# Performance work log

Hardware: AMD Instinct MI355X
Metric: run time of the kernel (lower is better)

The kernel has to match this reference:

```python
import jax, jax.numpy as jnp
import numpy as np


def setup_inputs() -> dict:
    key = jax.random.key(0)
    ks = jax.random.split(key, 8)
    Dm, E, N, R, K = 1024, 2048, 16, 64, 3
    s = 0.02
    x = jax.random.normal(ks[0], (2, 2048, Dm), jnp.float32)
    W_in = jax.random.normal(ks[1], (2 * E, Dm), jnp.float32) * s
    conv_w = jax.random.normal(ks[2], (E, 1, K), jnp.float32) * 0.1
    conv_b = jnp.zeros((E,), jnp.float32)
    W_sel = jax.random.normal(ks[3], (R + 2 * N, E), jnp.float32) * s
    dt_w = jax.random.normal(ks[4], (E, R), jnp.float32) * (R ** -0.5)
    dt_b = jax.random.normal(ks[5], (E,), jnp.float32) * 0.5
    A_log = jnp.log(jnp.tile(jnp.arange(1, N + 1, dtype=jnp.float32)[None, :], (E, 1)))
    D_param = jnp.ones((E,), jnp.float32)
    W_out = jax.random.normal(ks[6], (Dm, E), jnp.float32) * s
    return dict(x=x, W_in=W_in, conv_w=conv_w, conv_b=conv_b, W_sel=W_sel,
                dt_w=dt_w, dt_b=dt_b, A_log=A_log, D_param=D_param, W_out=W_out)


def reference(x, W_in, conv_w, conv_b, W_sel, dt_w, dt_b, A_log, D_param, W_out):
    Bsz, L, Dm = x.shape
    E = W_in.shape[0] // 2
    N = A_log.shape[1]
    R = dt_w.shape[1]
    K = conv_w.shape[-1]

    # input projection -> x, z
    xz = jnp.einsum('bld,ed->ble', x, W_in)          # [B,L,2E]
    xc, z = jnp.split(xz, 2, axis=-1)                # [B,L,E] each

    # causal depthwise conv1d + SiLU
    xt = xc.transpose(0, 2, 1)                       # [B,E,L]
    u = jax.lax.conv_general_dilated(
        xt, conv_w, window_strides=(1,), padding=[(K - 1, 0)],
        feature_group_count=E, dimension_numbers=('NCH', 'OIH', 'NCH'))
    u = jax.nn.silu(u + conv_b[None, :, None]).transpose(0, 2, 1)  # [B,L,E]

    # selective projection -> dt (low rank), B, C
    dbc = jnp.einsum('ble,re->blr', u, W_sel)        # [B,L,R+2N]
    dt_low, Bm, Cm = jnp.split(dbc, [R, R + N], axis=-1)
    delta = jax.nn.softplus(jnp.einsum('blr,er->ble', dt_low, dt_w) + dt_b)  # [B,L,E]

    A = -jnp.exp(A_log)                              # [E,N]

    def step(h, inp):
        d_t, u_t, B_t, C_t = inp                     # [B,E],[B,E],[B,N],[B,N]
        dA = jnp.exp(d_t[..., None] * A)             # [B,E,N]
        h = dA * h + (d_t * u_t)[..., None] * B_t[:, None, :]
        y_t = jnp.einsum('ben,bn->be', h, C_t)
        return h, y_t

    h0 = jnp.zeros((Bsz, E, N), x.dtype)
    seq = (delta.transpose(1, 0, 2), u.transpose(1, 0, 2),
           Bm.transpose(1, 0, 2), Cm.transpose(1, 0, 2))
    _, ys = jax.lax.scan(step, h0, seq)              # ys: [L,B,E]

    y = ys.transpose(1, 0, 2) + u * D_param          # skip term D*u
    y = y * jax.nn.silu(z)                           # gating
    return jnp.einsum('ble,de->bld', y, W_out)       # [B,L,Dm]
```

## Files before the change

### kernel.cpp

```cpp
#include <hip/hip_runtime.h>
#include <cstdint>
#include <cstddef>

typedef unsigned short ushort_t;
typedef __bf16 bf16x8 __attribute__((ext_vector_type(8)));
typedef float f32x4 __attribute__((ext_vector_type(4)));
typedef unsigned short us8v __attribute__((ext_vector_type(8)));

#define TSZ   4096
#define LSEQ  2048
#define DM    1024
#define EE    2048
#define NST   16
#define RR    64
#define NC    64
#define CL    32
#define BE    4096
#define NSPLIT 16
#define NSPLIT4 2

__device__ __forceinline__ ushort_t f2bf(float f) {
  uint32_t u = __builtin_bit_cast(uint32_t, f);
  u = (u + 0x7FFFu + ((u >> 16) & 1u)) >> 16;
  return (ushort_t)u;
}
__device__ __forceinline__ float bf2f(ushort_t h) {
  uint32_t u = ((uint32_t)h) << 16;
  return __builtin_bit_cast(float, u);
}

__device__ __forceinline__ size_t paddr(int r, int k, int logK) {
  return ((size_t)(r >> 7) << (7 + logK)) + (size_t)(((k >> 5) << 12) +
         (((k >> 3) & 3) << 10) + ((r & 127) << 3) + (k & 7));
}
__device__ __forceinline__ size_t src_of(int j, int logK) {
  int rt = j >> (7 + logK);
  int rem = j & ((1 << (7 + logK)) - 1);
  int kp = rem >> 12;
  int kc = (rem >> 10) & 3;
  int rr = (rem >> 3) & 127;
  int k0 = rem & 7;
  return ((size_t)(rt * 128 + rr) << logK) + (kp << 5) + (kc << 3) + k0;
}

#define NX_  (TSZ * DM)
#define NWI_ (2 * EE * DM)
#define NDT_ (EE * RR)
#define NWO_ (DM * EE)
#define NWS_ (128 * EE)
#define NCVT (NX_ + NWI_ + NDT_ + NWO_ + NWS_)

__device__ __forceinline__ void cvt8(const float* __restrict__ src, ushort_t* __restrict__ dst,
                                     int j, int logK) {
  size_t s = src_of(j, logK);
  float4 a = *(const float4*)(src + s);
  float4 b = *(const float4*)(src + s + 4);
  us8v v;
  v[0] = f2bf(a.x); v[1] = f2bf(a.y); v[2] = f2bf(a.z); v[3] = f2bf(a.w);
  v[4] = f2bf(b.x); v[5] = f2bf(b.y); v[6] = f2bf(b.z); v[7] = f2bf(b.w);
  *(us8v*)(dst + j) = v;
}

__global__ void cvt_all_kernel(const float* __restrict__ x, const float* __restrict__ W_in,
                               const float* __restrict__ dt_w, const float* __restrict__ W_out,
                               const float* __restrict__ W_sel,
                               ushort_t* __restrict__ xb, ushort_t* __restrict__ wib,
                               ushort_t* __restrict__ dtwb, ushort_t* __restrict__ woutb,
                               ushort_t* __restrict__ wselb) {
  int j = (blockIdx.x * 256 + threadIdx.x) * 8;
  if (j < NX_) { cvt8(x, xb, j, 10); return; }
  j -= NX_;
  if (j < NWI_) { cvt8(W_in, wib, j, 10); return; }
  j -= NWI_;
  if (j < NDT_) { cvt8(dt_w, dtwb, j, 6); return; }
  j -= NDT_;
  if (j < NWO_) { cvt8(W_out, woutb, j, 11); return; }
  j -= NWO_;
  if (j < NWS_) {
    size_t s = src_of(j, 11);
    int row = (int)(s >> 11);
    us8v v;
    if (row < 96) {
      float4 a = *(const float4*)(W_sel + s);
      float4 b = *(const float4*)(W_sel + s + 4);
      v[0] = f2bf(a.x); v[1] = f2bf(a.y); v[2] = f2bf(a.z); v[3] = f2bf(a.w);
      v[4] = f2bf(b.x); v[5] = f2bf(b.y); v[6] = f2bf(b.z); v[7] = f2bf(b.w);
    } else {
      v = (us8v)0;
    }
    *(us8v*)(wselb + j) = v;
  }
}

__device__ __forceinline__ void stage4(const ushort_t* g, ushort_t* lds, int tid) {
#pragma unroll
  for (int s = 0; s < 4; s++)
    __builtin_amdgcn_global_load_lds(
        (const __attribute__((address_space(1))) unsigned int*)(g + (tid + 256 * s) * 8),
        (__attribute__((address_space(3))) unsigned int*)(lds + (tid + 256 * s) * 8), 16, 0, 0);
}

__global__ __launch_bounds__(256) void gemm_bt2_kernel(
    const ushort_t* __restrict__ A, const ushort_t* __restrict__ B, int K, int ksplit,
    float* __restrict__ Cf, int ldcf, ushort_t* __restrict__ Cb, int ldcb,
    const float* __restrict__ bias, int nvalid, int mode) {
  __shared__ __align__(16) ushort_t lA[2][128 * 64];
  const int tid = threadIdx.x;
  const int mtile = blockIdx.x, ntile = blockIdx.y;

  const size_t abase = (size_t)mtile * 128 * K;
  const size_t bbase = (size_t)ntile * 128 * K;
  const int lane = tid & 63, w = tid >> 6;
  const int wm = (w >> 1) * 64, wn = (w & 1) * 64;
  const int lr = lane & 15, quad = lane >> 4;

  auto loadB = [&](bf16x8 (&dst)[2][4], const ushort_t* pbase) {
#pragma unroll
    for (int kk = 0; kk < 2; kk++)
#pragma unroll
      for (int ni = 0; ni < 4; ni++)
        dst[kk][ni] = *(const bf16x8*)(pbase + (size_t)(kk * 512 + quad * 128 + wn + ni * 16 + lr) * 8);
  };

  f32x4 acc[4][4];
#pragma unroll
  for (int i = 0; i < 4; i++)
#pragma unroll
    for (int j = 0; j < 4; j++) acc[i][j] = (f32x4){0.f, 0.f, 0.f, 0.f};

  const int kstart = blockIdx.z * ksplit;
  const int nIter = (ksplit ? ksplit : K) >> 6;

  stage4(A + abase + (size_t)kstart * 128, lA[0], tid);
  bf16x8 bcur[2][4];
  loadB(bcur, B + bbase + (size_t)kstart * 128);

#pragma unroll 2
  for (int i = 0; i < nIter; ++i) {
    const int knext = (i + 1 < nIter) ? (kstart + (i + 1) * 64) : kstart;
    __asm__ volatile("s_barrier" ::: "memory");
    stage4(A + abase + (size_t)knext * 128, lA[(i + 1) & 1], tid);
    bf16x8 bnx[2][4];
    loadB(bnx, B + bbase + (size_t)knext * 128);
    __asm__ volatile("s_waitcnt vmcnt(12)" ::: "memory");
    __asm__ volatile("s_barrier" ::: "memory");
    const ushort_t* lab = lA[i & 1];
#pragma unroll
    for (int kk = 0; kk < 2; kk++) {
      bf16x8 af[4];
#pragma unroll
      for (int mi = 0; mi < 4; mi++)
        af[mi] = *(const bf16x8*)&lab[(kk * 512 + quad * 128 + wm + mi * 16 + lr) * 8];
#pragma unroll
      for (int mi = 0; mi < 4; mi++)
#pragma unroll
        for (int ni = 0; ni < 4; ni++)
          acc[mi][ni] = __builtin_amdgcn_mfma_f32_16x16x32_bf16(af[mi], bcur[kk][ni], acc[mi][ni], 0, 0, 0);
    }
#pragma unroll
    for (int kk = 0; kk < 2; kk++)
#pragma unroll
      for (int ni = 0; ni < 4; ni++)
        bcur[kk][ni] = bnx[kk][ni];
  }
  __asm__ volatile("s_waitcnt vmcnt(0)" ::: "memory");

  float* Cfp = (mode == 4) ? (Cf + (size_t)blockIdx.z * TSZ * ldcf) : Cf;
  const int grow0 = mtile * 128 + wm + quad * 4;
  const int gcol0 = ntile * 128 + wn + lr;
#pragma unroll
  for (int mi = 0; mi < 4; mi++) {
#pragma unroll
    for (int ni = 0; ni < 4; ni++) {
      int gcol = gcol0 + ni * 16;
      if (gcol >= nvalid) continue;
#pragma unroll
      for (int reg = 0; reg < 4; reg++) {
        int grow = grow0 + mi * 16 + reg;
        float v = acc[mi][ni][reg];
        if (mode == 1) {
          Cb[(size_t)grow * ldcb + gcol] = f2bf(v);
        } else if (mode == 5) {
          float t = v + bias[gcol];
          float sp = fmaxf(t, 0.f) + __logf(1.f + __expf(-fabsf(t)));
          ((_Float16*)Cb)[(size_t)grow * ldcb + gcol] = (_Float16)sp;
        } else if (mode == 6) {
          atomicAdd(&Cf[(size_t)grow * ldcf + gcol], v);
        } else {
          Cfp[(size_t)grow * ldcf + gcol] = v;
        }
      }
    }
  }
}

__global__ void reduce_dbc_kernel(const float* __restrict__ pbuf,
                                  float* __restrict__ bcbuf, ushort_t* __restrict__ dtlb) {
  int i = blockIdx.x * 256 + threadIdx.x;
  int t = i >> 7, col = i & 127;
  if (col >= 96) return;
  float s = 0.f;
#pragma unroll
  for (int p = 0; p < NSPLIT; p++) s += pbuf[(size_t)p * TSZ * 128 + i];
  if (col < 64) dtlb[paddr(t, col, 6)] = f2bf(s);
  else bcbuf[(size_t)t * 32 + (col - 64)] = s;
}

__global__ void conv_silu_kernel(const ushort_t* __restrict__ xzb,
                                 const float* __restrict__ conv_w,
                                 const float* __restrict__ conv_b,
                                 ushort_t* __restrict__ ub) {
  int j = (blockIdx.x * 256 + threadIdx.x) * 8;
  int rt = j >> 18;
  int rem = j & 262143;
  int e0 = ((rem >> 12) << 5) + (((rem >> 10) & 3) << 3);
  int t = rt * 128 + ((rem >> 3) & 127);
  int l = t & (LSEQ - 1);
  const ushort_t* r2 = xzb + (size_t)t * 4096 + e0;
  us8v x2 = *(const us8v*)r2;
  float acc[8];
#pragma unroll
  for (int q = 0; q < 8; q++)
    acc[q] = fmaf(conv_w[(e0 + q) * 3 + 2], bf2f(x2[q]), conv_b[e0 + q]);
  if (l >= 1) {
    us8v x1 = *(const us8v*)(r2 - 4096);
#pragma unroll
    for (int q = 0; q < 8; q++) acc[q] = fmaf(conv_w[(e0 + q) * 3 + 1], bf2f(x1[q]), acc[q]);
  }
  if (l >= 2) {
    us8v x0 = *(const us8v*)(r2 - 8192);
#pragma unroll
    for (int q = 0; q < 8; q++) acc[q] = fmaf(conv_w[(e0 + q) * 3 + 0], bf2f(x0[q]), acc[q]);
  }
  us8v o;
#pragma unroll
  for (int q = 0; q < 8; q++) {
    float s = acc[q] / (1.f + __expf(-acc[q]));
    o[q] = f2bf(s);
  }
  *(us8v*)(ub + j) = o;
}

__global__ void scan_passA_kernel(const _Float16* __restrict__ delta,
                                  const ushort_t* __restrict__ ub,
                                  const float* __restrict__ bcbuf,
                                  _Float16* __restrict__ chunk_h,
                                  float* __restrict__ chunk_sd) {
  const int c = blockIdx.y;
  const int bblk = blockIdx.x >> 3;
  const int tg0 = bblk * LSEQ + c * CL;
  const int be = blockIdx.x * 256 + threadIdx.x;
  const int e = be & (EE - 1);
  float h[NST];
#pragma unroll
  for (int n = 0; n < NST; n++) h[n] = 0.f;
  float sd = 0.f;
  size_t ub0 = paddr(tg0, e, 11);
  const float* __restrict__ bcrow = bcbuf + (size_t)tg0 * 32;
  for (int i = 0; i < CL; i++) {
    int tg = tg0 + i;
    float d = (float)delta[(size_t)tg * EE + e];
    float u = bf2f(ub[ub0 + i * 8]);
    float Bn[NST];
    *(float4*)&Bn[0]  = *(const float4*)(bcrow + 0);
    *(float4*)&Bn[4]  = *(const float4*)(bcrow + 4);
    *(float4*)&Bn[8]  = *(const float4*)(bcrow + 8);
    *(float4*)&Bn[12] = *(const float4*)(bcrow + 12);
    bcrow += 32;
    float r = __expf(-d);
    float wdu = d * u;
    float p = 1.f;
#pragma unroll
    for (int n = 0; n < NST; n++) {
      p *= r;
      h[n] = fmaf(p, h[n], wdu * Bn[n]);
    }
    sd += d;
  }
  size_t o = ((size_t)c * BE + be) * NST;
#pragma unroll
  for (int n = 0; n < NST; n++) chunk_h[o + n] = (_Float16)h[n];
  chunk_sd[(size_t)c * BE + be] = sd;
}

__global__ void combine_kernel(const _Float16* __restrict__ chunk_h,
                               const float* __restrict__ chunk_sd,
                               _Float16* __restrict__ hstart) {
  int gid = blockIdx.x * 256 + threadIdx.x;
  int be = gid >> 4, n = gid & 15;
  float hs = 0.f;
  float np1 = (float)(n + 1);
  for (int c = 0; c < NC; c++) {
    hstart[(size_t)c * BE * NST + gid] = (_Float16)hs;
    float sdv = chunk_sd[c * BE + be];
    float P = __expf(-np1 * sdv);
    hs = fmaf(P, hs, (float)chunk_h[(size_t)c * BE * NST + gid]);
  }
}

__global__ void scan_passC_kernel(const _Float16* __restrict__ delta,
                                  const ushort_t* __restrict__ ub,
                                  const ushort_t* __restrict__ xzb,
                                  const float* __restrict__ bcbuf,
                                  const _Float16* __restrict__ hstart,
                                  const float* __restrict__ D_param,
                                  ushort_t* __restrict__ gated) {
  const int c = blockIdx.y;
  const int bblk = blockIdx.x >> 3;
  const int tg0 = bblk * LSEQ + c * CL;
  const int be = blockIdx.x * 256 + threadIdx.x;
  const int e = be & (EE - 1);
  float h[NST];
  size_t ho = ((size_t)c * BE + be) * NST;
#pragma unroll
  for (int n = 0; n < NST; n++) h[n] = (float)hstart[ho + n];
  float Dp = D_param[e];
  size_t pk0 = paddr(tg0, e, 11);
  const float* __restrict__ bcrow = bcbuf + (size_t)tg0 * 32;
  for (int i = 0; i < CL; i++) {
    int tg = tg0 + i;
    float d = (float)delta[(size_t)tg * EE + e];
    float u = bf2f(ub[pk0 + i * 8]);
    float z = bf2f(xzb[(size_t)tg * 4096 + 2048 + e]);
    float Bn[NST], Cn[NST];
    *(float4*)&Bn[0]  = *(const float4*)(bcrow + 0);
    *(float4*)&Bn[4]  = *(const float4*)(bcrow + 4);
    *(float4*)&Bn[8]  = *(const float4*)(bcrow + 8);
    *(float4*)&Bn[12] = *(const float4*)(bcrow + 12);
    *(float4*)&Cn[0]  = *(const float4*)(bcrow + 16);
    *(float4*)&Cn[4]  = *(const float4*)(bcrow + 20);
    *(float4*)&Cn[8]  = *(const float4*)(bcrow + 24);
    *(float4*)&Cn[12] = *(const float4*)(bcrow + 28);
    bcrow += 32;
    float r = __expf(-d);
    float wdu = d * u;
    float p = 1.f, y = 0.f;
#pragma unroll
    for (int n = 0; n < NST; n++) {
      p *= r;
      h[n] = fmaf(p, h[n], wdu * Bn[n]);
      y = fmaf(h[n], Cn[n], y);
    }
    y = fmaf(u, Dp, y);
    float sz = z / (1.f + __expf(-z));
    gated[pk0 + i * 8] = f2bf(y * sz);
  }
}

extern "C" void kernel_launch(void* const* d_in, const int* in_sizes, int n_in,
                              void* d_out, int out_size, void* d_ws, size_t ws_size,
                              hipStream_t stream) {
  const float* x       = (const float*)d_in[0];
  const float* W_in    = (const float*)d_in[1];
  const float* conv_w  = (const float*)d_in[2];
  const float* conv_b  = (const float*)d_in[3];
  const float* W_sel   = (const float*)d_in[4];
  const float* dt_w    = (const float*)d_in[5];
  const float* dt_b    = (const float*)d_in[6];
  const float* D_param = (const float*)d_in[8];
  const float* W_out   = (const float*)d_in[9];
  float* out = (float*)d_out;

  char* ws = (char*)d_ws;
  size_t off = 0;
  auto alloc = [&](size_t bytes) -> void* {
    void* p = ws + off;
    off += (bytes + 255) & ~(size_t)255;
    return p;
  };
  ushort_t* xzb   = (ushort_t*)alloc((size_t)TSZ * 4096 * 2);
  ushort_t* ubuf  = (ushort_t*)alloc((size_t)TSZ * EE * 2);
  ushort_t* wselb = (ushort_t*)alloc((size_t)128 * EE * 2);
  ushort_t* dtwb  = (ushort_t*)alloc((size_t)EE * RR * 2);
  ushort_t* woutb = (ushort_t*)alloc((size_t)DM * EE * 2);
  float*    bcbuf = (float*)alloc((size_t)TSZ * 32 * 4);
  ushort_t* dtlb  = (ushort_t*)alloc((size_t)TSZ * RR * 2);
  float*    dscr  = (float*)alloc((size_t)TSZ * EE * 4);
  float*    csd   = (float*)alloc((size_t)NC * BE * 4);
  ushort_t* gated = (ushort_t*)alloc((size_t)TSZ * EE * 2);
  ushort_t* xb    = (ushort_t*)alloc((size_t)TSZ * DM * 2);
  ushort_t* wib   = (ushort_t*)alloc((size_t)(2 * EE) * DM * 2);
  _Float16* delta = (_Float16*)dscr;
  _Float16* chunk_h = (_Float16*)gated;
  _Float16* hstart  = (_Float16*)wib;
  float* pbuf2   = dscr;

  hipMemsetAsync(out, 0, (size_t)TSZ * DM * 4, stream);

  cvt_all_kernel<<<(NCVT / 8 + 255) / 256, 256, 0, stream>>>(x, W_in, dt_w, W_out, W_sel,
                                                             xb, wib, dtwb, woutb, wselb);

  gemm_bt2_kernel<<<dim3(32, 32), 256, 0, stream>>>(
      xb, wib, DM, 0, nullptr, 0, xzb, 4096, nullptr, 4096, 1);

  conv_silu_kernel<<<(TSZ * EE / 8) / 256, 256, 0, stream>>>(xzb, conv_w, conv_b, ubuf);

  gemm_bt2_kernel<<<dim3(32, 1, NSPLIT), 256, 0, stream>>>(
      ubuf, wselb, EE, EE / NSPLIT, pbuf2, 128, nullptr, 0, nullptr, 96, 4);
  reduce_dbc_kernel<<<(TSZ * 128) / 256, 256, 0, stream>>>(pbuf2, bcbuf, dtlb);

  gemm_bt2_kernel<<<dim3(32, 16), 256, 0, stream>>>(
      dtlb, dtwb, RR, 0, nullptr, 0, (ushort_t*)delta, EE, dt_b, EE, 5);

  scan_passA_kernel<<<dim3(BE / 256, NC), 256, 0, stream>>>(delta, ubuf, bcbuf, chunk_h, csd);
  combine_kernel<<<(BE * NST) / 256, 256, 0, stream>>>(chunk_h, csd, hstart);
  scan_passC_kernel<<<dim3(BE / 256, NC), 256, 0, stream>>>(delta, ubuf, xzb, bcbuf, hstart,
                                                            D_param, gated);

  gemm_bt2_kernel<<<dim3(32, 8, NSPLIT4), 256, 0, stream>>>(
      gated, woutb, EE, EE / NSPLIT4, out, DM, nullptr, 0, nullptr, DM, 6);
}
```

Measured before the change: 323.9 us.

## Replace atomic split-K output with partial buffers and reduction kernel; halve dbc split

```diff
diff --git a/kernel.cpp b/kernel.cpp
--- a/kernel.cpp
+++ b/kernel.cpp
@@ -16,7 +16,7 @@
 #define NC    64
 #define CL    32
 #define BE    4096
-#define NSPLIT 16
+#define NSPLIT 8
 #define NSPLIT4 2
 
 __device__ __forceinline__ ushort_t f2bf(float f) {
@@ -100,7 +100,7 @@
         (__attribute__((address_space(3))) unsigned int*)(lds + (tid + 256 * s) * 8), 16, 0, 0);
 }
 
-__global__ __launch_bounds__(256) void gemm_bt2_kernel(
+__global__ __launch_bounds__(256) void gemm_pipe_kernel(
     const ushort_t* __restrict__ A, const ushort_t* __restrict__ B, int K, int ksplit,
     float* __restrict__ Cf, int ldcf, ushort_t* __restrict__ Cb, int ldcb,
     const float* __restrict__ bias, int nvalid, int mode) {
@@ -114,12 +114,13 @@
   const int wm = (w >> 1) * 64, wn = (w & 1) * 64;
   const int lr = lane & 15, quad = lane >> 4;
 
-  auto loadB = [&](bf16x8 (&dst)[2][4], const ushort_t* pbase) {
+  bf16x8 breg[2][2][4];
+  auto loadB = [&](int buf, const ushort_t* pbase) {
 #pragma unroll
     for (int kk = 0; kk < 2; kk++)
 #pragma unroll
       for (int ni = 0; ni < 4; ni++)
-        dst[kk][ni] = *(const bf16x8*)(pbase + (size_t)(kk * 512 + quad * 128 + wn + ni * 16 + lr) * 8);
+        breg[buf][kk][ni] = *(const bf16x8*)(pbase + (size_t)(kk * 512 + quad * 128 + wn + ni * 16 + lr) * 8);
   };
 
   f32x4 acc[4][4];
@@ -132,16 +133,14 @@
   const int nIter = (ksplit ? ksplit : K) >> 6;
 
   stage4(A + abase + (size_t)kstart * 128, lA[0], tid);
-  bf16x8 bcur[2][4];
-  loadB(bcur, B + bbase + (size_t)kstart * 128);
+  loadB(0, B + bbase + (size_t)kstart * 128);
 
 #pragma unroll 2
   for (int i = 0; i < nIter; ++i) {
     const int knext = (i + 1 < nIter) ? (kstart + (i + 1) * 64) : kstart;
     __asm__ volatile("s_barrier" ::: "memory");
     stage4(A + abase + (size_t)knext * 128, lA[(i + 1) & 1], tid);
-    bf16x8 bnx[2][4];
-    loadB(bnx, B + bbase + (size_t)knext * 128);
+    loadB((i + 1) & 1, B + bbase + (size_t)knext * 128);
     __asm__ volatile("s_waitcnt vmcnt(12)" ::: "memory");
     __asm__ volatile("s_barrier" ::: "memory");
     const ushort_t* lab = lA[i & 1];
@@ -155,13 +154,8 @@
       for (int mi = 0; mi < 4; mi++)
 #pragma unroll
         for (int ni = 0; ni < 4; ni++)
-          acc[mi][ni] = __builtin_amdgcn_mfma_f32_16x16x32_bf16(af[mi], bcur[kk][ni], acc[mi][ni], 0, 0, 0);
+          acc[mi][ni] = __builtin_amdgcn_mfma_f32_16x16x32_bf16(af[mi], breg[i & 1][kk][ni], acc[mi][ni], 0, 0, 0);
     }
-#pragma unroll
-    for (int kk = 0; kk < 2; kk++)
-#pragma unroll
-      for (int ni = 0; ni < 4; ni++)
-        bcur[kk][ni] = bnx[kk][ni];
   }
   __asm__ volatile("s_waitcnt vmcnt(0)" ::: "memory");
 
@@ -184,8 +178,6 @@
           float t = v + bias[gcol];
           float sp = fmaxf(t, 0.f) + __logf(1.f + __expf(-fabsf(t)));
           ((_Float16*)Cb)[(size_t)grow * ldcb + gcol] = (_Float16)sp;
-        } else if (mode == 6) {
-          atomicAdd(&Cf[(size_t)grow * ldcf + gcol], v);
         } else {
           Cfp[(size_t)grow * ldcf + gcol] = v;
         }
@@ -204,6 +196,14 @@
   for (int p = 0; p < NSPLIT; p++) s += pbuf[(size_t)p * TSZ * 128 + i];
   if (col < 64) dtlb[paddr(t, col, 6)] = f2bf(s);
   else bcbuf[(size_t)t * 32 + (col - 64)] = s;
+}
+
+__global__ void reduce_out_kernel(const float* __restrict__ pbuf, float* __restrict__ out) {
+  int i = blockIdx.x * 256 + threadIdx.x;
+  float s = pbuf[i];
+#pragma unroll
+  for (int p = 1; p < NSPLIT4; p++) s += pbuf[(size_t)p * TSZ * DM + i];
+  out[i] = s;
 }
 
 __global__ void conv_silu_kernel(const ushort_t* __restrict__ xzb,
@@ -384,22 +384,21 @@
   _Float16* chunk_h = (_Float16*)gated;
   _Float16* hstart  = (_Float16*)wib;
   float* pbuf2   = dscr;
-
-  hipMemsetAsync(out, 0, (size_t)TSZ * DM * 4, stream);
+  float* pbuf4   = dscr;
 
   cvt_all_kernel<<<(NCVT / 8 + 255) / 256, 256, 0, stream>>>(x, W_in, dt_w, W_out, W_sel,
                                                              xb, wib, dtwb, woutb, wselb);
 
-  gemm_bt2_kernel<<<dim3(32, 32), 256, 0, stream>>>(
+  gemm_pipe_kernel<<<dim3(32, 32), 256, 0, stream>>>(
       xb, wib, DM, 0, nullptr, 0, xzb, 4096, nullptr, 4096, 1);
 
   conv_silu_kernel<<<(TSZ * EE / 8) / 256, 256, 0, stream>>>(xzb, conv_w, conv_b, ubuf);
 
-  gemm_bt2_kernel<<<dim3(32, 1, NSPLIT), 256, 0, stream>>>(
+  gemm_pipe_kernel<<<dim3(32, 1, NSPLIT), 256, 0, stream>>>(
       ubuf, wselb, EE, EE / NSPLIT, pbuf2, 128, nullptr, 0, nullptr, 96, 4);
   reduce_dbc_kernel<<<(TSZ * 128) / 256, 256, 0, stream>>>(pbuf2, bcbuf, dtlb);
 
-  gemm_bt2_kernel<<<dim3(32, 16), 256, 0, stream>>>(
+  gemm_pipe_kernel<<<dim3(32, 16), 256, 0, stream>>>(
       dtlb, dtwb, RR, 0, nullptr, 0, (ushort_t*)delta, EE, dt_b, EE, 5);
 
   scan_passA_kernel<<<dim3(BE / 256, NC), 256, 0, stream>>>(delta, ubuf, bcbuf, chunk_h, csd);
@@ -407,6 +406,7 @@
   scan_passC_kernel<<<dim3(BE / 256, NC), 256, 0, stream>>>(delta, ubuf, xzb, bcbuf, hstart,
                                                             D_param, gated);
 
-  gemm_bt2_kernel<<<dim3(32, 8, NSPLIT4), 256, 0, stream>>>(
-      gated, woutb, EE, EE / NSPLIT4, out, DM, nullptr, 0, nullptr, DM, 6);
-}
+  gemm_pipe_kernel<<<dim3(32, 8, NSPLIT4), 256, 0, stream>>>(
+      gated, woutb, EE, EE / NSPLIT4, pbuf4, DM, nullptr, 0, nullptr, DM, 4);
+  reduce_out_kernel<<<(TSZ * DM) / 256, 256, 0, stream>>>(pbuf4, out);
+}
```

Result: slower. 507.8 us (+56.8%).
